# Kernel tuning notes

Hardware: AMD Instinct MI355X
Metric: run time of the kernel (lower is better)

## Reference

```python
import jax, jax.numpy as jnp
import numpy as np

HEADS = 8
HEAD_DIM = 64
EPS = 1e-5


def setup_inputs() -> dict:
    key = jax.random.key(0)
    k1, k2, k3 = jax.random.split(key, 3)
    dim, hidden = 512, HEADS * HEAD_DIM
    x = jax.random.normal(k1, (8, dim, 64, 64), dtype=jnp.float32)
    w_qkv = jax.random.normal(k2, (hidden * 3, dim), dtype=jnp.float32) * (dim ** -0.5)
    w_out = jax.random.normal(k3, (dim, hidden), dtype=jnp.float32) * (hidden ** -0.5)
    b_out = jnp.zeros((dim,), dtype=jnp.float32)
    g = jnp.ones((dim,), dtype=jnp.float32)
    return {"x": x, "w_qkv": w_qkv, "w_out": w_out, "b_out": b_out, "g": g}


def reference(x, w_qkv, w_out, b_out, g):
    b, c, h, w = x.shape
    n = h * w
    scale = HEAD_DIM ** -0.5
    xf = x.reshape(b, c, n)  # 1x1 conv == channel matmul
    qkv = jnp.einsum('oc,bcn->bon', w_qkv, xf)
    q, k, v = jnp.split(qkv, 3, axis=1)
    def to_heads(t):
        return t.reshape(b, HEADS, HEAD_DIM, n)
    q, k, v = to_heads(q), to_heads(k), to_heads(v)
    q = jax.nn.softmax(q, axis=-2) * scale   # softmax over head_dim
    k = jax.nn.softmax(k, axis=-1)           # softmax over tokens
    v = v / n
    # context: (B,H,d,d) = k (B,H,d,N) @ v^T (B,H,N,e)
    context = jnp.einsum('bhdn,bhen->bhde', k, v)
    # out: context^T (e,d) @ q (d,N) -> (B,H,e,N)
    out = jnp.einsum('bhde,bhdn->bhen', context, q)
    out = out.reshape(b, HEADS * HEAD_DIM, n)
    y = jnp.einsum('co,bon->bcn', w_out, out) + b_out[None, :, None]
    # channel LayerNorm (mean/var over dim=1, biased var, scale g only)
    mean = jnp.mean(y, axis=1, keepdims=True)
    var = jnp.var(y, axis=1, keepdims=True)
    y = (y - mean) * jax.lax.rsqrt(var + EPS) * g[None, :, None]
    return y.reshape(b, c, h, w)
```

## Files before the change

kernel.cpp:

```cpp
#include <hip/hip_runtime.h>
#include <math.h>

#define BB 8
#define NN 4096
#define CD 512
#define HH 8
#define DD 64
#define OC3 1536
#define NSPLIT 16

typedef _Float16 f16;
typedef _Float16 half8 __attribute__((ext_vector_type(8)));
typedef _Float16 half4v __attribute__((ext_vector_type(4)));
typedef float f32x4 __attribute__((ext_vector_type(4)));

__device__ __forceinline__ void gload_lds16(const void* g, void* l) {
    __builtin_amdgcn_global_load_lds(
        (const __attribute__((address_space(1))) unsigned int*)g,
        (__attribute__((address_space(3))) unsigned int*)l, 16, 0, 0);
}

__global__ __launch_bounds__(256) void split_w_kernel(
    const float* __restrict__ w, f16* __restrict__ wh, f16* __restrict__ wl)
{
    int idx = blockIdx.x * 256 + threadIdx.x;
    float4 v = ((const float4*)w)[idx];
    float a[4] = {v.x, v.y, v.z, v.w};
    half4v h, l;
    #pragma unroll
    for (int i = 0; i < 4; ++i) {
        float s = a[i] * 64.f;
        f16 hh = (f16)s;
        h[i] = hh;
        l[i] = (f16)(s - (float)hh);
    }
    *(half4v*)(&wh[(long)idx * 4]) = h;
    *(half4v*)(&wl[(long)idx * 4]) = l;
}

__global__ __launch_bounds__(256) void split_x_kernel(
    const float* __restrict__ x, f16* __restrict__ xth, f16* __restrict__ xtl)
{
    __shared__ float tile[64][65];
    int b = blockIdx.z;
    int n0 = blockIdx.x * 64, c0 = blockIdx.y * 64;
    const float* xb = x + ((long)b * CD + c0) * NN + n0;
    int t = threadIdx.x;
    int tr = t >> 6, tc = t & 63;
    #pragma unroll
    for (int i = 0; i < 16; ++i)
        tile[tr + i * 4][tc] = xb[(long)(tr + i * 4) * NN + tc];
    __syncthreads();

    int nl = t >> 3, ck = (t & 7) * 8;
    long obase = ((long)b * NN + n0) * CD + c0;
    #pragma unroll
    for (int p = 0; p < 2; ++p) {
        int n = nl + p * 32;
        half8 h, l;
        #pragma unroll
        for (int j = 0; j < 8; ++j) {
            float s = tile[ck + j][n] * 16.f;
            f16 hv = (f16)s;
            h[j] = hv;
            l[j] = (f16)(s - (float)hv);
        }
        *(half8*)(&xth[obase + (long)n * CD + ck]) = h;
        *(half8*)(&xtl[obase + (long)n * CD + ck]) = l;
    }
}

#define AR  16384
#define BUF 65536

#define STAGE(Lb, k0s)  do {                                                   \
    long kb_ = (long)(k0s) * 2;                                                \
    _Pragma("unroll")                                                          \
    for (int c_ = 0; c_ < 2; ++c_) {                                           \
        long rowoff_ = (long)(rb0 + c_ * 16) * 1024;                           \
        long ldsoff_ = (long)(rb0 + c_ * 16) * 64;                             \
        gload_lds16(gA_h + rowoff_ + kb_ + g_lane, (Lb) + 0 * AR + ldsoff_);   \
        gload_lds16(gA_l + rowoff_ + kb_ + g_lane, (Lb) + 1 * AR + ldsoff_);   \
        gload_lds16(gB_h + rowoff_ + kb_ + g_lane, (Lb) + 2 * AR + ldsoff_);   \
        gload_lds16(gB_l + rowoff_ + kb_ + g_lane, (Lb) + 3 * AR + ldsoff_);   \
    } } while (0)

__global__ __launch_bounds__(512, 2) void mfma_gemm_kernel(
    const f16* __restrict__ Ah, const f16* __restrict__ Al, long sA,
    const f16* __restrict__ Bh, const f16* __restrict__ Bl, long sB,
    float* __restrict__ Cp, long sC, int ldC, float base_sc)
{
    __shared__ f16 lds[2][4][256 * 32];
    int bz = blockIdx.z;
    int n0 = blockIdx.x * 256, m0 = blockIdx.y * 256;
    int t = threadIdx.x;
    int lane = t & 63, wid = t >> 6;
    int wy = wid >> 2, wx = wid & 3;

    int cl = (lane & 3) ^ ((lane >> 3) & 3);
    long g_lane = (long)(lane >> 2) * 1024 + (long)cl * 16;

    const char* gA_h = (const char*)(Ah + bz * sA) + (long)m0 * 1024;
    const char* gA_l = (const char*)(Al + bz * sA) + (long)m0 * 1024;
    const char* gB_h = (const char*)(Bh + bz * sB) + (long)n0 * 1024;
    const char* gB_l = (const char*)(Bl + bz * sB) + (long)n0 * 1024;

    char* L0 = (char*)&lds[0][0][0];
    int rb0 = wid * 32;

    int cp = (lane >> 4) ^ (((lane & 15) >> 1) & 3);
    long offA = (long)(wy * 128 + (lane & 15)) * 64 + (long)cp * 16;
    long offB = (long)(wx * 64 + (lane & 15)) * 64 + (long)cp * 16;

    f32x4 acc[8][4];
    #pragma unroll
    for (int i = 0; i < 8; ++i)
        #pragma unroll
        for (int j = 0; j < 4; ++j)
            acc[i][j] = (f32x4){0.f, 0.f, 0.f, 0.f};

    STAGE(L0, 0);
    asm volatile("s_waitcnt vmcnt(0)" ::: "memory");
    __syncthreads();

    for (int s = 0; s < 16; ++s) {
        char* Lc = L0 + ((s & 1) ? BUF : 0);
        if (s < 15) {
            char* Ln = L0 + (((s + 1) & 1) ? BUF : 0);
            STAGE(Ln, (s + 1) * 32);
        }

        half8 ah[8], al[8];
        #pragma unroll
        for (int i = 0; i < 8; ++i) {
            ah[i] = *(const half8*)(Lc + 0 * AR + offA + i * 1024);
            al[i] = *(const half8*)(Lc + 1 * AR + offA + i * 1024);
        }
        #pragma unroll
        for (int j = 0; j < 4; ++j) {
            half8 bh = *(const half8*)(Lc + 2 * AR + offB + j * 1024);
            half8 bl = *(const half8*)(Lc + 3 * AR + offB + j * 1024);
            #pragma unroll
            for (int i = 0; i < 8; ++i) {
                acc[i][j] = __builtin_amdgcn_mfma_f32_16x16x32_f16(ah[i], bh, acc[i][j], 0, 0, 0);
                acc[i][j] = __builtin_amdgcn_mfma_f32_16x16x32_f16(ah[i], bl, acc[i][j], 0, 0, 0);
                acc[i][j] = __builtin_amdgcn_mfma_f32_16x16x32_f16(al[i], bh, acc[i][j], 0, 0, 0);
            }
        }

        asm volatile("s_waitcnt vmcnt(0)" ::: "memory");
        __syncthreads();
    }

    int colb = n0 + wx * 64 + (lane & 15);
    int rowb = m0 + wy * 128 + ((lane >> 4) << 2);

    if (m0 < 512) {
        int h0 = (m0 >> 6) + wy * 2;
        f16* qh_b = (f16*)(Cp + (long)bz * sC);
        f16* ql_b = qh_b + (long)CD * NN;
        #pragma unroll
        for (int i = 0; i < 8; ++i)
            #pragma unroll
            for (int j = 0; j < 4; ++j)
                #pragma unroll
                for (int r = 0; r < 4; ++r)
                    acc[i][j][r] *= base_sc;
        #pragma unroll
        for (int j = 0; j < 4; ++j) {
            long nj = colb + j * 16;
            #pragma unroll
            for (int g = 0; g < 2; ++g) {
                float mx = -INFINITY;
                #pragma unroll
                for (int di = 0; di < 4; ++di)
                    #pragma unroll
                    for (int r = 0; r < 4; ++r)
                        mx = fmaxf(mx, acc[g * 4 + di][j][r]);
                mx = fmaxf(mx, __shfl_xor(mx, 16));
                mx = fmaxf(mx, __shfl_xor(mx, 32));
                float sum = 0.f;
                #pragma unroll
                for (int di = 0; di < 4; ++di)
                    #pragma unroll
                    for (int r = 0; r < 4; ++r) {
                        float e = expf(acc[g * 4 + di][j][r] - mx);
                        acc[g * 4 + di][j][r] = e;
                        sum += e;
                    }
                sum += __shfl_xor(sum, 16);
                sum += __shfl_xor(sum, 32);
                float rj = 32.f / sum;
                long off = nj * CD + (h0 + g) * 64 + ((lane >> 4) << 2);
                #pragma unroll
                for (int di = 0; di < 4; ++di) {
                    half4v hh, ll;
                    #pragma unroll
                    for (int r = 0; r < 4; ++r) {
                        float v = acc[g * 4 + di][j][r] * rj;
                        f16 hv = (f16)v;
                        hh[r] = hv;
                        ll[r] = (f16)(v - (float)hv);
                    }
                    *(half4v*)(qh_b + off + di * 16) = hh;
                    *(half4v*)(ql_b + off + di * 16) = ll;
                }
            }
        }
        return;
    }

    if (m0 >= 1024) {
        f16* vhp = (f16*)(Cp + (long)bz * sC + 2L * CD * NN);
        f16* vlp = vhp + (long)CD * NN;
        float vsc = base_sc * 16.f;
        #pragma unroll
        for (int i = 0; i < 8; ++i)
            #pragma unroll
            for (int j = 0; j < 4; ++j)
                #pragma unroll
                for (int r = 0; r < 4; ++r) {
                    long row = rowb + i * 16 + r - 1024;
                    float val = acc[i][j][r] * vsc;
                    f16 hv = (f16)val;
                    vhp[row * NN + colb + j * 16] = hv;
                    vlp[row * NN + colb + j * 16] = (f16)(val - (float)hv);
                }
        return;
    }

    float* outp = Cp + bz * sC;
    #pragma unroll
    for (int i = 0; i < 8; ++i)
        #pragma unroll
        for (int j = 0; j < 4; ++j)
            #pragma unroll
            for (int r = 0; r < 4; ++r) {
                int row = rowb + i * 16 + r;
                outp[(long)row * ldC + colb + j * 16] = acc[i][j][r] * base_sc;
            }
}

#define AR2  8192
#define BUF2 32768

#define STAGE2(Lb, k0s)  do {                                                  \
    long kb_ = (long)(k0s) * 2;                                                \
    _Pragma("unroll")                                                          \
    for (int c_ = 0; c_ < 2; ++c_) {                                           \
        long rowoff_ = (long)(rb0 + c_ * 16) * 1024;                           \
        long ldsoff_ = (long)(rb0 + c_ * 16) * 64;                             \
        gload_lds16(gA_h + rowoff_ + kb_ + g_lane, (Lb) + 0 * AR2 + ldsoff_);  \
        gload_lds16(gA_l + rowoff_ + kb_ + g_lane, (Lb) + 1 * AR2 + ldsoff_);  \
        gload_lds16(gB_h + rowoff_ + kb_ + g_lane, (Lb) + 2 * AR2 + ldsoff_);  \
        gload_lds16(gB_l + rowoff_ + kb_ + g_lane, (Lb) + 3 * AR2 + ldsoff_);  \
    } } while (0)

__global__ __launch_bounds__(256) void mfma_gemm128_kernel(
    const f16* __restrict__ Ah, const f16* __restrict__ Al, long sA,
    const f16* __restrict__ Bh, const f16* __restrict__ Bl, long sB,
    float* __restrict__ Cp, long sC, int ldC,
    const float* __restrict__ bias, const float* __restrict__ inv_sc,
    float base_sc)
{
    __shared__ f16 lds[2][4][128 * 32];
    int bz = blockIdx.z;
    int n0 = blockIdx.x * 128, m0 = blockIdx.y * 128;
    int t = threadIdx.x;
    int lane = t & 63, wid = t >> 6;
    int wy = wid >> 1, wx = wid & 1;

    int cl = (lane & 3) ^ ((lane >> 3) & 3);
    long g_lane = (long)(lane >> 2) * 1024 + (long)cl * 16;

    const char* gA_h = (const char*)(Ah + bz * sA) + (long)m0 * 1024;
    const char* gA_l = (const char*)(Al + bz * sA) + (long)m0 * 1024;
    const char* gB_h = (const char*)(Bh + bz * sB) + (long)n0 * 1024;
    const char* gB_l = (const char*)(Bl + bz * sB) + (long)n0 * 1024;

    char* L0 = (char*)&lds[0][0][0];
    int rb0 = wid * 32;

    int cp = (lane >> 4) ^ (((lane & 15) >> 1) & 3);
    long offA = (long)(wy * 64 + (lane & 15)) * 64 + (long)cp * 16;
    long offB = (long)(wx * 64 + (lane & 15)) * 64 + (long)cp * 16;

    f32x4 acc[4][4];
    #pragma unroll
    for (int i = 0; i < 4; ++i)
        #pragma unroll
        for (int j = 0; j < 4; ++j)
            acc[i][j] = (f32x4){0.f, 0.f, 0.f, 0.f};

    STAGE2(L0, 0);
    asm volatile("s_waitcnt vmcnt(0)" ::: "memory");
    __syncthreads();

    for (int s = 0; s < 16; ++s) {
        char* Lc = L0 + ((s & 1) ? BUF2 : 0);
        if (s < 15) {
            char* Ln = L0 + (((s + 1) & 1) ? BUF2 : 0);
            STAGE2(Ln, (s + 1) * 32);
        }

        half8 ah[4], al[4], bh[4], bl[4];
        #pragma unroll
        for (int i = 0; i < 4; ++i) {
            ah[i] = *(const half8*)(Lc + 0 * AR2 + offA + i * 1024);
            al[i] = *(const half8*)(Lc + 1 * AR2 + offA + i * 1024);
            bh[i] = *(const half8*)(Lc + 2 * AR2 + offB + i * 1024);
            bl[i] = *(const half8*)(Lc + 3 * AR2 + offB + i * 1024);
        }
        #pragma unroll
        for (int i = 0; i < 4; ++i)
            #pragma unroll
            for (int j = 0; j < 4; ++j) {
                acc[i][j] = __builtin_amdgcn_mfma_f32_16x16x32_f16(ah[i], bh[j], acc[i][j], 0, 0, 0);
                acc[i][j] = __builtin_amdgcn_mfma_f32_16x16x32_f16(ah[i], bl[j], acc[i][j], 0, 0, 0);
                acc[i][j] = __builtin_amdgcn_mfma_f32_16x16x32_f16(al[i], bh[j], acc[i][j], 0, 0, 0);
            }

        asm volatile("s_waitcnt vmcnt(0)" ::: "memory");
        __syncthreads();
    }

    int colb = n0 + wx * 64 + (lane & 15);
    int rowb = m0 + wy * 64 + ((lane >> 4) << 2);
    float* outp = Cp + bz * sC;
    float mult = base_sc * (inv_sc ? inv_sc[bz] : 1.f);
    #pragma unroll
    for (int i = 0; i < 4; ++i)
        #pragma unroll
        for (int j = 0; j < 4; ++j)
            #pragma unroll
            for (int r = 0; r < 4; ++r) {
                int row = rowb + i * 16 + r;
                float bb = bias ? bias[row] : 0.f;
                outp[(long)row * ldC + colb + j * 16] = acc[i][j][r] * mult + bb;
            }
}

__global__ __launch_bounds__(256) void softmax_k_kernel(
    const float* __restrict__ qkv, f16* __restrict__ ksp)
{
    int row = blockIdx.x;
    int b = row >> 9;
    int hd = row & (CD - 1);
    const float* base = qkv + ((long)b * OC3 + CD + hd) * NN;
    f16* khb = ksp + (long)b * 2 * CD * NN + (long)hd * NN;
    f16* klb = khb + (long)CD * NN;
    int t = threadIdx.x;

    float v[16];
    #pragma unroll
    for (int i = 0; i < 16; ++i) v[i] = base[t + i * 256];

    __shared__ float red[256];
    float mx = -INFINITY;
    #pragma unroll
    for (int i = 0; i < 16; ++i) mx = fmaxf(mx, v[i]);
    red[t] = mx; __syncthreads();
    for (int off = 128; off > 0; off >>= 1) {
        if (t < off) red[t] = fmaxf(red[t], red[t + off]);
        __syncthreads();
    }
    mx = red[0]; __syncthreads();

    float s = 0.f;
    #pragma unroll
    for (int i = 0; i < 16; ++i) {
        v[i] = expf(v[i] - mx);
        s += v[i];
    }
    red[t] = s; __syncthreads();
    for (int off = 128; off > 0; off >>= 1) {
        if (t < off) red[t] += red[t + off];
        __syncthreads();
    }
    float inv = 4096.f / red[0];

    #pragma unroll
    for (int i = 0; i < 16; ++i) {
        float val = v[i] * inv;
        f16 hv = (f16)val;
        khb[t + i * 256] = hv;
        klb[t + i * 256] = (f16)(val - (float)hv);
    }
}

__global__ __launch_bounds__(256) void ctx_mfma_kernel(
    const f16* __restrict__ ksp, const float* __restrict__ qkv,
    float* __restrict__ ctxp)
{
    __shared__ f16 lds[4][64 * 32];
    int sp = blockIdx.x;
    int bh = blockIdx.y;
    int b = bh >> 3, h = bh & 7;
    int t = threadIdx.x, lane = t & 63, w = t >> 6;

    const char* khg = (const char*)(ksp + (long)b * 2 * CD * NN) + (long)h * 64 * (NN * 2);
    const char* klg = khg + (long)CD * NN * 2;
    const char* vhg = (const char*)(qkv + ((long)b * OC3 + 2L * CD) * NN) + (long)h * 64 * (NN * 2);
    const char* vlg = vhg + (long)CD * NN * 2;
    const char* gw = (w == 0) ? khg : (w == 1) ? klg : (w == 2) ? vhg : vlg;

    int cl = (lane & 3) ^ ((lane >> 3) & 3);
    char* larr = (char*)&lds[0][0] + w * 4096;
    char* L = (char*)&lds[0][0];
    int cp16 = ((lane >> 4) ^ (((lane & 15) >> 1) & 3)) * 16;
    int lr = lane & 15;

    f32x4 acc[4];
    #pragma unroll
    for (int i = 0; i < 4; ++i) acc[i] = (f32x4){0.f, 0.f, 0.f, 0.f};

    for (int ks = 0; ks < 8; ++ks) {
        long kbyte = ((long)sp * 256 + ks * 32) * 2;
        #pragma unroll
        for (int c = 0; c < 4; ++c)
            gload_lds16(gw + (long)(c * 16 + (lane >> 2)) * (NN * 2) + kbyte + (long)cl * 16,
                        larr + c * 1024 + lane * 16);
        asm volatile("s_waitcnt vmcnt(0)" ::: "memory");
        __syncthreads();

        half8 ah[4], al[4], bhf, blf;
        #pragma unroll
        for (int i = 0; i < 4; ++i) {
            ah[i] = *(const half8*)(L + 0 * 4096 + (i * 16 + lr) * 64 + cp16);
            al[i] = *(const half8*)(L + 1 * 4096 + (i * 16 + lr) * 64 + cp16);
        }
        bhf = *(const half8*)(L + 2 * 4096 + (w * 16 + lr) * 64 + cp16);
        blf = *(const half8*)(L + 3 * 4096 + (w * 16 + lr) * 64 + cp16);
        #pragma unroll
        for (int i = 0; i < 4; ++i) {
            acc[i] = __builtin_amdgcn_mfma_f32_16x16x32_f16(ah[i], bhf, acc[i], 0, 0, 0);
            acc[i] = __builtin_amdgcn_mfma_f32_16x16x32_f16(ah[i], blf, acc[i], 0, 0, 0);
            acc[i] = __builtin_amdgcn_mfma_f32_16x16x32_f16(al[i], bhf, acc[i], 0, 0, 0);
        }
        __syncthreads();
    }

    float* op = ctxp + ((long)bh * NSPLIT + sp) * 4096;
    #pragma unroll
    for (int i = 0; i < 4; ++i)
        #pragma unroll
        for (int r = 0; r < 4; ++r)
            op[(i * 16 + (lane >> 4) * 4 + r) * 64 + w * 16 + lr] = acc[i][r];
}

__global__ __launch_bounds__(256) void context_reduce_kernel(
    const float* __restrict__ ctxp, float* __restrict__ ctx)
{
    int idx = blockIdx.x * 256 + threadIdx.x;
    int bh = idx >> 12;
    int de = idx & 4095;
    double s = 0.0;
    #pragma unroll
    for (int sp = 0; sp < NSPLIT; ++sp)
        s += (double)ctxp[((long)bh * NSPLIT + sp) * 4096 + de];
    ctx[idx] = (float)(s * (1.0 / 268435456.0));
}

__global__ __launch_bounds__(256) void fold_wout_kernel(
    const float* __restrict__ w_out, const float* __restrict__ ctx,
    float* __restrict__ Mf)
{
    __shared__ float cl[64][65];
    int ct = blockIdx.x;
    int bh = blockIdx.y;
    int b = bh >> 3, h = bh & 7;
    int t = threadIdx.x;
    const float* cp = ctx + (long)bh * 4096;
    #pragma unroll
    for (int i = 0; i < 16; ++i) {
        int o = t + i * 256;
        cl[o >> 6][o & 63] = cp[o];
    }
    __syncthreads();

    int d = t & 63, tc = t >> 6;
    #pragma unroll 4
    for (int ci = 0; ci < 32; ++ci) {
        int c = ct * 128 + tc * 32 + ci;
        const float* wr = w_out + (long)c * CD + h * DD;
        float s = 0.f;
        #pragma unroll
        for (int e = 0; e < 64; ++e) s += wr[e] * cl[d][e];
        Mf[((long)b * CD + c) * CD + h * DD + d] = s;
    }
}

__global__ __launch_bounds__(256) void max_m_part_kernel(
    const float* __restrict__ Mf, float* __restrict__ part)
{
    int blk = blockIdx.x;
    int b = blk >> 5, sub = blk & 31;
    const float4* p = (const float4*)(Mf + (long)b * CD * CD) + (long)sub * 2048;
    float mx = 0.f;
    for (int i = threadIdx.x; i < 2048; i += 256) {
        float4 v = p[i];
        mx = fmaxf(mx, fmaxf(fmaxf(fabsf(v.x), fabsf(v.y)),
                             fmaxf(fabsf(v.z), fabsf(v.w))));
    }
    __shared__ float red[256];
    red[threadIdx.x] = mx; __syncthreads();
    for (int off = 128; off > 0; off >>= 1) {
        if (threadIdx.x < off) red[threadIdx.x] = fmaxf(red[threadIdx.x], red[threadIdx.x + off]);
        __syncthreads();
    }
    if (threadIdx.x == 0) part[blk] = red[0];
}

__global__ __launch_bounds__(64) void max_m_final_kernel(
    const float* __restrict__ part, float* __restrict__ scl)
{
    int b = threadIdx.x;
    if (b < 8) {
        float m = 0.f;
        #pragma unroll
        for (int i = 0; i < 32; ++i) m = fmaxf(m, part[b * 32 + i]);
        int e = (m > 1e-30f) ? ilogbf(m) : 0;
        scl[b] = ldexpf(1.f, 10 - e);
        scl[8 + b] = ldexpf(1.f, e - 10);
    }
}

__global__ __launch_bounds__(256) void split_m_kernel(
    const float* __restrict__ Mf, const float* __restrict__ scl,
    f16* __restrict__ mh, f16* __restrict__ ml)
{
    int idx = blockIdx.x * 256 + threadIdx.x;
    float s = scl[idx >> 16];
    float4 v = ((const float4*)Mf)[idx];
    float a[4] = {v.x, v.y, v.z, v.w};
    half4v h, l;
    #pragma unroll
    for (int i = 0; i < 4; ++i) {
        float tval = a[i] * s;
        f16 hv = (f16)tval;
        h[i] = hv;
        l[i] = (f16)(tval - (float)hv);
    }
    *(half4v*)(&mh[(long)idx * 4]) = h;
    *(half4v*)(&ml[(long)idx * 4]) = l;
}

__global__ __launch_bounds__(256) void layernorm_kernel(
    const float* __restrict__ qkv, const float* __restrict__ g,
    float* __restrict__ out)
{
    int t = threadIdx.x;
    int tn = t & 31, cy = t >> 5;
    long col = (long)blockIdx.x * 32 + tn;
    int n = (int)(col & (NN - 1));
    int b = (int)(col >> 12);
    const float* base = qkv + (long)b * OC3 * NN + (long)CD * NN + n;

    float v[64];
    double s = 0.0, ss = 0.0;
    #pragma unroll
    for (int i = 0; i < 64; ++i) {
        v[i] = base[(long)(cy * 64 + i) * NN];
        s += (double)v[i];
        ss += (double)v[i] * (double)v[i];
    }

    __shared__ double rs[8][32], rss[8][32];
    rs[cy][tn] = s; rss[cy][tn] = ss;
    __syncthreads();
    __shared__ float mb[32], ib[32];
    if (cy == 0) {
        double S = 0.0, SS = 0.0;
        #pragma unroll
        for (int j = 0; j < 8; ++j) { S += rs[j][tn]; SS += rss[j][tn]; }
        double mean = S * (1.0 / CD);
        double var = SS * (1.0 / CD) - mean * mean;
        mb[tn] = (float)mean;
        ib[tn] = (float)(1.0 / sqrt(var + 1e-5));
    }
    __syncthreads();
    float m = mb[tn], iv = ib[tn];

    float* oc = out + (long)b * CD * NN + n;
    #pragma unroll
    for (int i = 0; i < 64; ++i)
        oc[(long)(cy * 64 + i) * NN] = (v[i] - m) * iv * g[cy * 64 + i];
}

extern "C" void kernel_launch(void* const* d_in, const int* in_sizes, int n_in,
                              void* d_out, int out_size, void* d_ws, size_t ws_size,
                              hipStream_t stream)
{
    const float* x     = (const float*)d_in[0];
    const float* w_qkv = (const float*)d_in[1];
    const float* w_out = (const float*)d_in[2];
    const float* b_out = (const float*)d_in[3];
    const float* g     = (const float*)d_in[4];
    float* out = (float*)d_out;

    float* ws   = (float*)d_ws;
    float* qkv  = ws;
    float* ctxp = qkv + (long)BB * OC3 * NN;
    float* ctx  = ctxp + (long)BB * HH * NSPLIT * DD * DD;
    f16*   mh   = (f16*)(ctx + (long)BB * HH * DD * DD);
    f16*   ml   = mh + (long)BB * CD * CD;
    f16*   wh   = (f16*)(ml + (long)BB * CD * CD);
    f16*   wl   = wh + (long)OC3 * CD;
    float* scl  = (float*)(wl + (long)OC3 * CD);
    float* part = scl + 16;
    float* Mf   = ctxp;

    f16* xth = (f16*)d_out;
    f16* xtl = xth + (long)BB * NN * CD;
    f16* ksp = (f16*)d_out;

    split_w_kernel<<<(OC3 * CD / 4) / 256, 256, 0, stream>>>(w_qkv, wh, wl);
    split_x_kernel<<<dim3(NN / 64, CD / 64, BB), 256, 0, stream>>>(x, xth, xtl);

    mfma_gemm_kernel<<<dim3(NN / 256, OC3 / 256, BB), 512, 0, stream>>>(
        wh, wl, 0L, xth, xtl, (long)NN * CD,
        qkv, (long)OC3 * NN, NN, 1.0f / 1024.0f);

    softmax_k_kernel<<<BB * CD, 256, 0, stream>>>(qkv, ksp);

    ctx_mfma_kernel<<<dim3(NSPLIT, BB * HH), 256, 0, stream>>>(ksp, qkv, ctxp);
    context_reduce_kernel<<<(BB * HH * DD * DD) / 256, 256, 0, stream>>>(ctxp, ctx);

    fold_wout_kernel<<<dim3(4, BB * HH), 256, 0, stream>>>(w_out, ctx, Mf);
    max_m_part_kernel<<<256, 256, 0, stream>>>(Mf, part);
    max_m_final_kernel<<<1, 64, 0, stream>>>(part, scl);
    split_m_kernel<<<(BB * CD * CD / 4) / 256, 256, 0, stream>>>(Mf, scl, mh, ml);

    mfma_gemm128_kernel<<<dim3(NN / 128, CD / 128, BB), 256, 0, stream>>>(
        mh, ml, (long)CD * CD,
        (const f16*)qkv, (const f16*)qkv + (long)CD * NN, (long)OC3 * NN * 2,
        qkv + (long)CD * NN, (long)OC3 * NN, NN, b_out, scl + 8, 1.0f / 256.0f);

    layernorm_kernel<<<(BB * NN) / 32, 256, 0, stream>>>(qkv, g, out);
}
```

Before: 381.3 us.

## Interleave prefetch loads with MFMA phases and raise wave priority during MFMA

Splits each k-step of the split-fp16 GEMM main loop into four phases. Each phase issues a slice of the next stage's global-to-LDS loads, reads two A fragments from LDS and runs their MFMAs under s_setprio(1). All B fragments are now loaded up front. The aim is to spread memory traffic across the compute and keep the matrix cores busy instead of issuing all prefetches at once. In exchange it adds three extra barriers per iteration and keeps more fragments live in registers.

After: 389.8 us. 2.2% more time.

```diff
diff --git a/kernel.cpp b/kernel.cpp
--- a/kernel.cpp
+++ b/kernel.cpp
@@ -85,6 +85,20 @@
         gload_lds16(gB_l + rowoff_ + kb_ + g_lane, (Lb) + 3 * AR + ldsoff_);   \
     } } while (0)
 
+#define PH_MFMA(I0) do {                                                       \
+    __builtin_amdgcn_s_setprio(1);                                             \
+    _Pragma("unroll")                                                          \
+    for (int j = 0; j < 4; ++j) {                                              \
+        acc[I0][j]     = __builtin_amdgcn_mfma_f32_16x16x32_f16(ah[I0], bh[j], acc[I0][j], 0, 0, 0);     \
+        acc[I0][j]     = __builtin_amdgcn_mfma_f32_16x16x32_f16(ah[I0], bl[j], acc[I0][j], 0, 0, 0);     \
+        acc[I0][j]     = __builtin_amdgcn_mfma_f32_16x16x32_f16(al[I0], bh[j], acc[I0][j], 0, 0, 0);     \
+        acc[I0+1][j]   = __builtin_amdgcn_mfma_f32_16x16x32_f16(ah[I0+1], bh[j], acc[I0+1][j], 0, 0, 0); \
+        acc[I0+1][j]   = __builtin_amdgcn_mfma_f32_16x16x32_f16(ah[I0+1], bl[j], acc[I0+1][j], 0, 0, 0); \
+        acc[I0+1][j]   = __builtin_amdgcn_mfma_f32_16x16x32_f16(al[I0+1], bh[j], acc[I0+1][j], 0, 0, 0); \
+    }                                                                           \
+    __builtin_amdgcn_s_setprio(0);                                              \
+} while (0)
+
 __global__ __launch_bounds__(512, 2) void mfma_gemm_kernel(
     const f16* __restrict__ Ah, const f16* __restrict__ Al, long sA,
     const f16* __restrict__ Bh, const f16* __restrict__ Bl, long sB,
@@ -125,29 +139,61 @@
 
     for (int s = 0; s < 16; ++s) {
         char* Lc = L0 + ((s & 1) ? BUF : 0);
-        if (s < 15) {
-            char* Ln = L0 + (((s + 1) & 1) ? BUF : 0);
-            STAGE(Ln, (s + 1) * 32);
-        }
-
-        half8 ah[8], al[8];
-        #pragma unroll
-        for (int i = 0; i < 8; ++i) {
-            ah[i] = *(const half8*)(Lc + 0 * AR + offA + i * 1024);
-            al[i] = *(const half8*)(Lc + 1 * AR + offA + i * 1024);
+        char* Ln = L0 + (((s + 1) & 1) ? BUF : 0);
+        bool pf = (s < 15);
+        long kbn = (long)(s + 1) * 64;
+        long row0 = (long)rb0 * 1024,      lds0 = (long)rb0 * 64;
+        long row1 = (long)(rb0 + 16) * 1024, lds1 = (long)(rb0 + 16) * 64;
+
+        half8 ah[8], al[8], bh[4], bl[4];
+
+        if (pf) {
+            gload_lds16(gA_h + row0 + kbn + g_lane, Ln + 0 * AR + lds0);
+            gload_lds16(gA_l + row0 + kbn + g_lane, Ln + 1 * AR + lds0);
         }
         #pragma unroll
         for (int j = 0; j < 4; ++j) {
-            half8 bh = *(const half8*)(Lc + 2 * AR + offB + j * 1024);
-            half8 bl = *(const half8*)(Lc + 3 * AR + offB + j * 1024);
-            #pragma unroll
-            for (int i = 0; i < 8; ++i) {
-                acc[i][j] = __builtin_amdgcn_mfma_f32_16x16x32_f16(ah[i], bh, acc[i][j], 0, 0, 0);
-                acc[i][j] = __builtin_amdgcn_mfma_f32_16x16x32_f16(ah[i], bl, acc[i][j], 0, 0, 0);
-                acc[i][j] = __builtin_amdgcn_mfma_f32_16x16x32_f16(al[i], bh, acc[i][j], 0, 0, 0);
-            }
-        }
-
+            bh[j] = *(const half8*)(Lc + 2 * AR + offB + j * 1024);
+            bl[j] = *(const half8*)(Lc + 3 * AR + offB + j * 1024);
+        }
+        ah[0] = *(const half8*)(Lc + 0 * AR + offA + 0 * 1024);
+        al[0] = *(const half8*)(Lc + 1 * AR + offA + 0 * 1024);
+        ah[1] = *(const half8*)(Lc + 0 * AR + offA + 1 * 1024);
+        al[1] = *(const half8*)(Lc + 1 * AR + offA + 1 * 1024);
+        PH_MFMA(0);
+        __syncthreads();
+
+        if (pf) {
+            gload_lds16(gB_h + row0 + kbn + g_lane, Ln + 2 * AR + lds0);
+            gload_lds16(gB_l + row0 + kbn + g_lane, Ln + 3 * AR + lds0);
+        }
+        ah[2] = *(const half8*)(Lc + 0 * AR + offA + 2 * 1024);
+        al[2] = *(const half8*)(Lc + 1 * AR + offA + 2 * 1024);
+        ah[3] = *(const half8*)(Lc + 0 * AR + offA + 3 * 1024);
+        al[3] = *(const half8*)(Lc + 1 * AR + offA + 3 * 1024);
+        PH_MFMA(2);
+        __syncthreads();
+
+        if (pf) {
+            gload_lds16(gA_h + row1 + kbn + g_lane, Ln + 0 * AR + lds1);
+            gload_lds16(gA_l + row1 + kbn + g_lane, Ln + 1 * AR + lds1);
+        }
+        ah[4] = *(const half8*)(Lc + 0 * AR + offA + 4 * 1024);
+        al[4] = *(const half8*)(Lc + 1 * AR + offA + 4 * 1024);
+        ah[5] = *(const half8*)(Lc + 0 * AR + offA + 5 * 1024);
+        al[5] = *(const half8*)(Lc + 1 * AR + offA + 5 * 1024);
+        PH_MFMA(4);
+        __syncthreads();
+
+        if (pf) {
+            gload_lds16(gB_h + row1 + kbn + g_lane, Ln + 2 * AR + lds1);
+            gload_lds16(gB_l + row1 + kbn + g_lane, Ln + 3 * AR + lds1);
+        }
+        ah[6] = *(const half8*)(Lc + 0 * AR + offA + 6 * 1024);
+        al[6] = *(const half8*)(Lc + 1 * AR + offA + 6 * 1024);
+        ah[7] = *(const half8*)(Lc + 0 * AR + offA + 7 * 1024);
+        al[7] = *(const half8*)(Lc + 1 * AR + offA + 7 * 1024);
+        PH_MFMA(6);
         asm volatile("s_waitcnt vmcnt(0)" ::: "memory");
         __syncthreads();
     }
```
